# Optimization experiments

Hardware: AMD Instinct MI355X
Metric: run time of the kernel (lower is better)

The kernel has to match this reference:

```python
import jax, jax.numpy as jnp
import numpy as np

K = 5  # k_for_maxpool
EPS_OH = 1.0 - 0.001


def _conv_block(x, W, b):
    # x: [N, L, D]; Conv1d(D, D, 3, padding=2), LeakyReLU(0.1), slice [1:1+L], residual
    L = x.shape[1]
    xc = jnp.swapaxes(x, 1, 2)  # [N, D, L]
    y = jax.lax.conv_general_dilated(xc, W, window_strides=(1,), padding=[(2, 2)],
                                     dimension_numbers=('NCH', 'OIH', 'NCH'))
    y = y + b[None, :, None]
    y = jax.nn.leaky_relu(y, 0.1)
    y = y[:, :, 1:1 + L]
    return jnp.swapaxes(y, 1, 2) + x


def _normalize(x):
    return x / jnp.linalg.norm(x, axis=-1, keepdims=True)


def _pool(sim):
    # sim: [..., Q, L] -> [..., Q, 3]: (max, mean of top-K, mean over all)
    s = jnp.sort(sim, axis=-1)
    kmax = s[..., -K:]
    return jnp.stack([kmax[..., -1], kmax.mean(-1), s.mean(-1)], axis=-1)


def setup_inputs() -> dict:
    key = jax.random.key(0)
    ks = jax.random.split(key, 16)
    S, L, Q, D = 4096, 64, 32, 300
    inp = {
        'doc_sents_embeds': jax.random.normal(ks[0], (S, L, D), jnp.float32),
        'question_embeds': jax.random.normal(ks[1], (Q, D), jnp.float32),
        'q_idfs': jax.random.uniform(ks[2], (Q, 1), jnp.float32),
        'sents_gaf': jax.random.uniform(ks[3], (S, 3), jnp.float32),
        'conv1_w': jax.random.normal(ks[4], (D, D, 3), jnp.float32) * 0.05,
        'conv1_b': jax.random.normal(ks[5], (D,), jnp.float32) * 0.05,
        'conv2_w': jax.random.normal(ks[6], (D, D, 3), jnp.float32) * 0.05,
        'conv2_b': jax.random.normal(ks[7], (D,), jnp.float32) * 0.05,
        'qw_w': jax.random.normal(ks[8], (1, D + 1), jnp.float32) * 0.05,
        'qw_b': jax.random.normal(ks[9], (1,), jnp.float32) * 0.05,
        'mlp1_w': jax.random.normal(ks[10], (8, 9), jnp.float32) * 0.3,
        'mlp1_b': jax.random.normal(ks[11], (8,), jnp.float32) * 0.05,
        'mlp2_w': jax.random.normal(ks[12], (1, 8), jnp.float32) * 0.3,
        'mlp2_b': jax.random.normal(ks[13], (1,), jnp.float32) * 0.05,
        'out_w': jax.random.normal(ks[14], (1, 4), jnp.float32) * 0.3,
    }
    return inp


def reference(doc_sents_embeds, question_embeds, q_idfs, sents_gaf,
              conv1_w, conv1_b, conv2_w, conv2_b,
              qw_w, qw_b, mlp1_w, mlp1_b, mlp2_w, mlp2_b, out_w):
    Q = question_embeds.shape[0]
    # question context (two trigram conv blocks)
    q_ctx = _conv_block(_conv_block(question_embeds[None], conv1_w, conv1_b),
                        conv2_w, conv2_b)[0]  # [Q, D]
    # question token weights
    qw_in = jnp.concatenate([q_ctx, q_idfs], axis=-1)  # [Q, D+1]
    q_weights = jax.nn.softmax((qw_in @ qw_w.T + qw_b)[:, 0], axis=-1)  # [Q]
    # sentence context features, vectorized over all sentences
    sent_ctx = _conv_block(_conv_block(doc_sents_embeds, conv1_w, conv1_b),
                           conv2_w, conv2_b)  # [S, L, D]
    # cosine similarity matrices: [S, Q, L]
    qn = _normalize(question_embeds)
    dn = _normalize(doc_sents_embeds)
    sim_insens = jnp.einsum('qd,sld->sql', qn, dn)
    sim_oh = (sim_insens > EPS_OH).astype(sim_insens.dtype)
    qcn = _normalize(q_ctx)
    scn = _normalize(sent_ctx)
    sim_sens = jnp.einsum('qd,sld->sql', qcn, scn)
    # pooled features: [S, Q, 9] (order: oh, insensitive, sensitive)
    pooled = jnp.concatenate([_pool(sim_oh), _pool(sim_insens), _pool(sim_sens)], axis=-1)
    lo = jax.nn.leaky_relu(pooled @ mlp1_w.T + mlp1_b, 0.1)
    lo = (lo @ mlp2_w.T + mlp2_b)[..., 0]  # [S, Q]
    sent_emit = (lo * q_weights[None, :]).sum(-1) / Q  # [S]
    feats = jnp.concatenate([sents_gaf, sent_emit[:, None]], axis=-1)  # [S, 4]
    return jax.nn.sigmoid(feats @ out_w[0])  # [S]
```

## Files before the change

kernel.cpp:

```cpp
#include <hip/hip_runtime.h>
#include <math.h>

typedef __attribute__((ext_vector_type(8))) short short8;
typedef __attribute__((ext_vector_type(4))) short short4_t;
typedef __attribute__((ext_vector_type(4))) float f32x4;

#define RS      312
#define SST     69
#define EPS_OH  0.999f

__device__ __forceinline__ float waveSum(float v) {
#pragma unroll
  for (int off = 32; off; off >>= 1) v += __shfl_xor(v, off);
  return v;
}
__device__ __forceinline__ float leaky(float x) { return fmaxf(x, 0.1f * x); }

__device__ __forceinline__ short f2b(float f) {
  unsigned u = __float_as_uint(f);
  unsigned r = (u + 0x7FFFu + ((u >> 16) & 1u)) >> 16;
  return (short)r;
}
__device__ __forceinline__ float b2f(short h) {
  return __uint_as_float(((unsigned)(unsigned short)h) << 16);
}

__global__ __launch_bounds__(256) void qconv_kernel(
    const float* __restrict__ x, const float* __restrict__ W,
    const float* __restrict__ b, float* __restrict__ y)
{
  int idx = blockIdx.x * 256 + threadIdx.x;
  if (idx >= 76800) return;
  int part = idx & 7, gid = idx >> 3;
  int o = gid % 300, l = gid / 300;
  const float* Wo = W + o * 900;
  float acc = 0.f;
  for (int i = part; i < 300; i += 8) {
    float x1 = x[l * 300 + i];
    float x0 = (l >= 1) ? x[(l - 1) * 300 + i] : 0.f;
    float x2 = (l <= 30) ? x[(l + 1) * 300 + i] : 0.f;
    acc += Wo[i * 3] * x0 + Wo[i * 3 + 1] * x1 + Wo[i * 3 + 2] * x2;
  }
  acc += __shfl_xor(acc, 1);
  acc += __shfl_xor(acc, 2);
  acc += __shfl_xor(acc, 4);
  if (part == 0) y[gid] = leaky(acc + b[o]) + x[gid];
}

__global__ __launch_bounds__(256) void qfinish_kernel(
    const float* __restrict__ qemb, const float* __restrict__ qctx,
    const float* __restrict__ qidf, const float* __restrict__ qww,
    const float* __restrict__ qwb,
    float* __restrict__ qwv, short* __restrict__ qf)
{
  __shared__ float inq[32], inqc[32], lg[32];
  int tid = threadIdx.x, lane = tid & 63, w = tid >> 6;
  int r = w * 8 + (lane >> 3), sub = lane & 7;
  float sq = 0.f, sqc = 0.f, dt = 0.f;
  for (int i = sub; i < 300; i += 8) {
    float a = qemb[r * 300 + i]; sq  += a * a;
    float c = qctx[r * 300 + i]; sqc += c * c;
    dt += c * qww[i];
  }
#pragma unroll
  for (int off = 4; off; off >>= 1) {
    sq  += __shfl_xor(sq, off);
    sqc += __shfl_xor(sqc, off);
    dt  += __shfl_xor(dt, off);
  }
  if (sub == 0) {
    inq[r] = rsqrtf(sq); inqc[r] = rsqrtf(sqc);
    lg[r] = dt + qidf[r] * qww[300] + qwb[0];
  }
  __syncthreads();
  if (w == 0) {
    float L = (lane < 32) ? lg[lane] : -1e30f;
    float m = L;
#pragma unroll
    for (int off = 32; off; off >>= 1) m = fmaxf(m, __shfl_xor(m, off));
    float e = (lane < 32) ? expf(L - m) : 0.f;
    float ssum = e;
#pragma unroll
    for (int off = 32; off; off >>= 1) ssum += __shfl_xor(ssum, off);
    if (lane < 32) qwv[lane] = e / ssum;
  }
  __syncthreads();
  for (int t = tid; t < 2560; t += 256) {
    int ln = t & 63;
    int rest = t >> 6;
    int kt = rest % 10; rest /= 10;
    int mt = rest & 1; int sflag = rest >> 1;
    const float* src  = sflag ? qctx : qemb;
    const float* innv = sflag ? inqc : inq;
    int q  = mt * 16 + (ln & 15);
    int i0 = kt * 32 + (ln >> 4) * 8;
    float iv = innv[q];
    short8 v;
#pragma unroll
    for (int j = 0; j < 8; ++j) {
      int i = i0 + j;
      v[j] = f2b((i < 300) ? src[q * 300 + i] * iv : 0.f);
    }
    *(short8*)(qf + (size_t)t * 8) = v;
  }
}

__global__ __launch_bounds__(256) void wfrag_kernel(
    const float* __restrict__ W, short* __restrict__ Wf)
{
  int t = blockIdx.x * 256 + threadIdx.x;
  if (t >= 38400) return;
  int lane = t & 63;
  int rest = t >> 6;
  int mt = rest % 20; rest /= 20;
  int kt = rest % 10; int tap = rest / 10;
  int o  = mt * 16 + (lane & 15);
  int i0 = kt * 32 + (lane >> 4) * 8;
  short8 v;
#pragma unroll
  for (int j = 0; j < 8; ++j) {
    int i = i0 + j;
    v[j] = f2b((o < 300 && i < 300) ? W[o * 900 + i * 3 + tap] : 0.f);
  }
  *(short8*)(Wf + (size_t)t * 8) = v;
}


__device__ __forceinline__ void pool_all(
    const float* SIMb, float* featb, int lane, int foff, bool do_oh)
{
  int q = lane >> 1, half = lane & 1;
  const float* p = SIMb + q * SST + half * 32;
  float t0 = -3e38f, t1 = -3e38f, t2 = -3e38f, t3 = -3e38f, t4 = -3e38f;
  float ssum = 0.f;
  int cnt = 0;
#pragma unroll
  for (int i = 0; i < 32; ++i) {
    float v = p[i];
    ssum += v;
    if (do_oh) cnt += (v > EPS_OH) ? 1 : 0;
    float m, c;
    m = fmaxf(t0, v); c = fminf(t0, v); t0 = m;
    m = fmaxf(t1, c); c = fminf(t1, c); t1 = m;
    m = fmaxf(t2, c); c = fminf(t2, c); t2 = m;
    m = fmaxf(t3, c); c = fminf(t3, c); t3 = m;
    t4 = fmaxf(t4, c);
  }
  float p0 = __shfl_xor(t0, 1), p1 = __shfl_xor(t1, 1), p2 = __shfl_xor(t2, 1),
        p3 = __shfl_xor(t3, 1), p4 = __shfl_xor(t4, 1);
  float s2 = __shfl_xor(ssum, 1);
  int   c2 = __shfl_xor(cnt, 1);
  float m0 = fmaxf(t0, p4), m1 = fmaxf(t1, p3), m2 = fmaxf(t2, p2),
        m3 = fmaxf(t3, p1), m4 = fmaxf(t4, p0);
  if (half == 0) {
    float tmax = fmaxf(t0, p0);
    float t5   = m0 + m1 + m2 + m3 + m4;
    float stot = ssum + s2;
    int   c    = cnt + c2;
    float* fq = featb + q * 9;
    if (do_oh) {
      fq[0] = (c > 0) ? 1.f : 0.f;
      fq[1] = (c < 5 ? (float)c : 5.f) * 0.2f;
      fq[2] = (float)c * (1.f / 64.f);
    }
    fq[foff + 0] = tmax;
    fq[foff + 1] = t5 * 0.2f;
    fq[foff + 2] = stot * (1.f / 64.f);
  }
}

__device__ __forceinline__ void conv_mfma_ip3(
    short* tb, const short* __restrict__ Wf,
    const float* __restrict__ bias, int w, int r, int g, int lane)
{
  f32x4 acc[2][4];
#pragma unroll
  for (int mi = 0; mi < 2; ++mi)
#pragma unroll
    for (int nt = 0; nt < 4; ++nt) acc[mi][nt] = (f32x4){0.f, 0.f, 0.f, 0.f};

  const int rm0 = (r == 0) ? 0 : (r - 1);
  const int rp3 = (r == 15) ? 63 : (49 + r);
  int rows[3][4];
  rows[0][0] = rm0;    rows[0][1] = 15 + r; rows[0][2] = 31 + r; rows[0][3] = 47 + r;
  rows[1][0] = r;      rows[1][1] = 16 + r; rows[1][2] = 32 + r; rows[1][3] = 48 + r;
  rows[2][0] = 1 + r;  rows[2][1] = 17 + r; rows[2][2] = 33 + r; rows[2][3] = rp3;

  const short* wl = Wf + (size_t)lane * 8 + (size_t)(2 * w) * 512;
  const int colg = g * 8;

  short8 afb[2][2], bfb[2][4];

#pragma unroll
  for (int mi = 0; mi < 2; ++mi)
    afb[0][mi] = *(const short8*)(wl + (size_t)mi * 512);
#pragma unroll
  for (int nt = 0; nt < 4; ++nt)
    bfb[0][nt] = *(const short8*)(tb + rows[0][nt] * RS + colg);

#pragma unroll
  for (int s = 0; s < 30; ++s) {
    const int kt = s / 3, tap = s % 3;
    const int cur = s & 1, nxt = cur ^ 1;
    if (s + 1 < 30) {
      const int kt2 = (s + 1) / 3, tap2 = (s + 1) % 3;
      const size_t afo = (size_t)((tap2 * 10 + kt2) * 20) * 512;
#pragma unroll
      for (int mi = 0; mi < 2; ++mi)
        afb[nxt][mi] = *(const short8*)(wl + afo + (size_t)mi * 512);
      const int col2 = kt2 * 32 + colg;
#pragma unroll
      for (int nt = 0; nt < 4; ++nt)
        bfb[nxt][nt] = *(const short8*)(tb + rows[tap2][nt] * RS + col2);
    }
    short8 f0 = bfb[cur][0], f1 = bfb[cur][1], f2 = bfb[cur][2], f3 = bfb[cur][3];
    if (tap == 0) f0 = (r == 0)  ? (short8)0 : f0;
    if (tap == 2) f3 = (r == 15) ? (short8)0 : f3;
#pragma unroll
    for (int mi = 0; mi < 2; ++mi) {
      short8 af = afb[cur][mi];
      acc[mi][0] = __builtin_amdgcn_mfma_f32_16x16x32_bf16(af, f0, acc[mi][0], 0, 0, 0);
      acc[mi][1] = __builtin_amdgcn_mfma_f32_16x16x32_bf16(af, f1, acc[mi][1], 0, 0, 0);
      acc[mi][2] = __builtin_amdgcn_mfma_f32_16x16x32_bf16(af, f2, acc[mi][2], 0, 0, 0);
      acc[mi][3] = __builtin_amdgcn_mfma_f32_16x16x32_bf16(af, f3, acc[mi][3], 0, 0, 0);
    }
  }

  f32x4 bv[2];
  short4_t resv[2][4];
#pragma unroll
  for (int mi = 0; mi < 2; ++mi) {
    const int m0 = (w * 2 + mi) * 16 + g * 4;
    if (m0 < 300) {
      bv[mi] = *(const f32x4*)(bias + m0);
#pragma unroll
      for (int nt = 0; nt < 4; ++nt)
        resv[mi][nt] = *(const short4_t*)(tb + (nt * 16 + r) * RS + m0);
    }
  }
  __syncthreads();
#pragma unroll
  for (int mi = 0; mi < 2; ++mi) {
    const int m0 = (w * 2 + mi) * 16 + g * 4;
    if (m0 < 300) {
#pragma unroll
      for (int nt = 0; nt < 4; ++nt) {
        int l = nt * 16 + r;
        short4_t outv;
#pragma unroll
        for (int j = 0; j < 4; ++j) {
          float a = acc[mi][nt][j] + bv[mi][j];
          a = leaky(a) + b2f(resv[mi][nt][j]);
          outv[j] = f2b(a);
        }
        *(short4_t*)(tb + l * RS + m0) = outv;
      }
    }
  }
}

__device__ __forceinline__ void sim_mfma(
    const short* src, const short* __restrict__ qf, const float* invn,
    float* SIMb, int ti, int r, int g, int lane)
{
  int smt = ti >> 2, snt = ti & 3;
  f32x4 acc = (f32x4){0.f, 0.f, 0.f, 0.f};
#pragma unroll
  for (int kt = 0; kt < 10; ++kt) {
    short8 bf = *(const short8*)(src + (snt * 16 + r) * RS + kt * 32 + g * 8);
    short8 af = *(const short8*)(qf + (size_t)((smt * 10 + kt) * 64 + lane) * 8);
    acc = __builtin_amdgcn_mfma_f32_16x16x32_bf16(af, bf, acc, 0, 0, 0);
  }
  int l = snt * 16 + r;
  float iv = invn[l];
#pragma unroll
  for (int j = 0; j < 4; ++j)
    SIMb[(smt * 16 + g * 4 + j) * SST + l] = acc[j] * iv;
}

__device__ __forceinline__ void norms_lds(const short* Xb, float* invn, int tid) {
  if (tid >= 512) return;
  int row = tid >> 3, part = tid & 7;
  float ssum = 0.f;
  for (int i = part * 8; i < 304; i += 64) {
    short8 hv = *(const short8*)(Xb + row * RS + i);
#pragma unroll
    for (int j = 0; j < 8; ++j) { float f = b2f(hv[j]); ssum += f * f; }
  }
  ssum += __shfl_xor(ssum, 1);
  ssum += __shfl_xor(ssum, 2);
  ssum += __shfl_xor(ssum, 4);
  if (part == 0) invn[row] = rsqrtf(ssum);
}

__global__ __launch_bounds__(640, 5) void sent_kernel(
    const float* __restrict__ doc, const short* __restrict__ qf,
    const float* __restrict__ qwv, const float* __restrict__ gaf,
    const short* __restrict__ Wf1, const float* __restrict__ b1,
    const short* __restrict__ Wf2, const float* __restrict__ b2,
    const float* __restrict__ m1w, const float* __restrict__ m1b,
    const float* __restrict__ m2w, const float* __restrict__ m2b,
    const float* __restrict__ ow, float* __restrict__ out)
{
  __shared__ short TB[64 * RS + 8];
  __shared__ float SIMb[32 * SST];
  __shared__ float invn[64];
  __shared__ float featb[288];

  const int tid = threadIdx.x, lane = tid & 63, w = tid >> 6;
  const int r = lane & 15, g = lane >> 4;
  const int s = blockIdx.x;

  if (tid >= 576) {
    short* p = TB + (tid - 576) * RS + 300;
    *(short4_t*)p = (short4_t)0;
    *(short8*)(p + 4) = (short8)0;
  } else if (tid == 575) {
    *(short8*)(TB + 64 * RS) = (short8)0;
  }
  if (tid < 512) {
    int l = tid >> 3, part = tid & 7;
    const float* xr = doc + (size_t)s * 19200 + l * 300;
    float ssum = 0.f;
#pragma unroll
    for (int m = 0; m < 5; ++m) {
      int c = part * 8 + m * 64;
      if (c <= 292) {
        f32x4 u0 = *(const f32x4*)(xr + c);
        f32x4 u1 = *(const f32x4*)(xr + c + 4);
        short8 o;
#pragma unroll
        for (int j = 0; j < 4; ++j) {
          ssum += u0[j] * u0[j] + u1[j] * u1[j];
          o[j] = f2b(u0[j]); o[4 + j] = f2b(u1[j]);
        }
        *(short8*)(TB + l * RS + c) = o;
      } else if (c == 296) {
        f32x4 u0 = *(const f32x4*)(xr + 296);
        short4_t o;
#pragma unroll
        for (int j = 0; j < 4; ++j) { ssum += u0[j] * u0[j]; o[j] = f2b(u0[j]); }
        *(short4_t*)(TB + l * RS + 296) = o;
      }
    }
    ssum += __shfl_xor(ssum, 1);
    ssum += __shfl_xor(ssum, 2);
    ssum += __shfl_xor(ssum, 4);
    if (part == 0) invn[l] = rsqrtf(ssum);
  }
  __syncthreads();

  if (w < 8) sim_mfma(TB, qf, invn, SIMb, w, r, g, lane);
  __syncthreads();

  if (w == 8) pool_all(SIMb, featb, lane, 3, true);
  __syncthreads();

  conv_mfma_ip3(TB, Wf1, b1, w, r, g, lane);
  __syncthreads();

  conv_mfma_ip3(TB, Wf2, b2, w, r, g, lane);
  __syncthreads();

  norms_lds(TB, invn, tid);
  __syncthreads();

  if (w < 8) sim_mfma(TB, qf + 10240, invn, SIMb, w, r, g, lane);
  __syncthreads();

  if (w == 9) pool_all(SIMb, featb, lane, 6, false);
  __syncthreads();

  if (w == 0) {
    float val = 0.f;
    if (lane < 32) {
      int q = lane;
      float o8 = m2b[0];
#pragma unroll
      for (int j = 0; j < 8; ++j) {
        float a = m1b[j];
#pragma unroll
        for (int f = 0; f < 9; ++f) a += m1w[j * 9 + f] * featb[q * 9 + f];
        a = leaky(a);
        o8 += m2w[j] * a;
      }
      val = o8 * qwv[q];
    }
    float tot = waveSum(val);
    if (lane == 0) {
      float emit = tot * (1.f / 32.f);
      float z = gaf[s * 3 + 0] * ow[0] + gaf[s * 3 + 1] * ow[1] +
                gaf[s * 3 + 2] * ow[2] + emit * ow[3];
      out[s] = 1.f / (1.f + expf(-z));
    }
  }
}

extern "C" void kernel_launch(void* const* d_in, const int* in_sizes, int n_in,
                              void* d_out, int out_size, void* d_ws, size_t ws_size,
                              hipStream_t stream)
{
  const float* doc  = (const float*)d_in[0];
  const float* qemb = (const float*)d_in[1];
  const float* qidf = (const float*)d_in[2];
  const float* gaf  = (const float*)d_in[3];
  const float* W1   = (const float*)d_in[4];
  const float* b1   = (const float*)d_in[5];
  const float* W2   = (const float*)d_in[6];
  const float* b2   = (const float*)d_in[7];
  const float* qww  = (const float*)d_in[8];
  const float* qwb  = (const float*)d_in[9];
  const float* m1w  = (const float*)d_in[10];
  const float* m1b  = (const float*)d_in[11];
  const float* m2w  = (const float*)d_in[12];
  const float* m2b  = (const float*)d_in[13];
  const float* ow   = (const float*)d_in[14];
  float* out = (float*)d_out;

  float* ws   = (float*)d_ws;
  float* qc1  = ws;
  float* qctx = ws + 9600;
  float* qwv  = ws + 19200;
  short* wsS  = (short*)(ws + 19232);
  short* Wf1  = wsS;
  short* Wf2  = wsS + 307200;
  short* qfS  = wsS + 614400;

  wfrag_kernel<<<150, 256, 0, stream>>>(W1, Wf1);
  wfrag_kernel<<<150, 256, 0, stream>>>(W2, Wf2);
  qconv_kernel<<<300, 256, 0, stream>>>(qemb, W1, b1, qc1);
  qconv_kernel<<<300, 256, 0, stream>>>(qc1, W2, b2, qctx);
  qfinish_kernel<<<1, 256, 0, stream>>>(qemb, qctx, qidf, qww, qwb, qwv, qfS);
  sent_kernel<<<4096, 640, 0, stream>>>(doc, qfS, qwv, gaf, Wf1, b1, Wf2, b2,
                                        m1w, m1b, m2w, m2b, ow, out);
}
```

Measured before the change: 545.2 us.

## Shrink sentence block to 8 waves with uneven conv M-tile split

Cuts the per-sentence block from 10 waves (640 threads) to 8 waves (512 threads). The 20 conv output M-tiles are now split so waves 0-2 take three tiles each and waves 3-7 take two, and the pooling passes move to waves 6 and 7. The aim is to remove two mostly idle waves and allow more blocks per CU. In exchange, the waves with three tiles hold more accumulator registers and take longer, which makes the conv stage imbalanced.

```diff
diff --git a/kernel.cpp b/kernel.cpp
--- a/kernel.cpp
+++ b/kernel.cpp
@@ -169,13 +169,14 @@
   }
 }
 
+template <int NMT>
 __device__ __forceinline__ void conv_mfma_ip3(
     short* tb, const short* __restrict__ Wf,
-    const float* __restrict__ bias, int w, int r, int g, int lane)
-{
-  f32x4 acc[2][4];
-#pragma unroll
-  for (int mi = 0; mi < 2; ++mi)
+    const float* __restrict__ bias, int base, int r, int g, int lane)
+{
+  f32x4 acc[NMT][4];
+#pragma unroll
+  for (int mi = 0; mi < NMT; ++mi)
 #pragma unroll
     for (int nt = 0; nt < 4; ++nt) acc[mi][nt] = (f32x4){0.f, 0.f, 0.f, 0.f};
 
@@ -186,13 +187,13 @@
   rows[1][0] = r;      rows[1][1] = 16 + r; rows[1][2] = 32 + r; rows[1][3] = 48 + r;
   rows[2][0] = 1 + r;  rows[2][1] = 17 + r; rows[2][2] = 33 + r; rows[2][3] = rp3;
 
-  const short* wl = Wf + (size_t)lane * 8 + (size_t)(2 * w) * 512;
+  const short* wl = Wf + (size_t)lane * 8 + (size_t)base * 512;
   const int colg = g * 8;
 
-  short8 afb[2][2], bfb[2][4];
-
-#pragma unroll
-  for (int mi = 0; mi < 2; ++mi)
+  short8 afb[2][NMT], bfb[2][4];
+
+#pragma unroll
+  for (int mi = 0; mi < NMT; ++mi)
     afb[0][mi] = *(const short8*)(wl + (size_t)mi * 512);
 #pragma unroll
   for (int nt = 0; nt < 4; ++nt)
@@ -206,7 +207,7 @@
       const int kt2 = (s + 1) / 3, tap2 = (s + 1) % 3;
       const size_t afo = (size_t)((tap2 * 10 + kt2) * 20) * 512;
 #pragma unroll
-      for (int mi = 0; mi < 2; ++mi)
+      for (int mi = 0; mi < NMT; ++mi)
         afb[nxt][mi] = *(const short8*)(wl + afo + (size_t)mi * 512);
       const int col2 = kt2 * 32 + colg;
 #pragma unroll
@@ -217,7 +218,7 @@
     if (tap == 0) f0 = (r == 0)  ? (short8)0 : f0;
     if (tap == 2) f3 = (r == 15) ? (short8)0 : f3;
 #pragma unroll
-    for (int mi = 0; mi < 2; ++mi) {
+    for (int mi = 0; mi < NMT; ++mi) {
       short8 af = afb[cur][mi];
       acc[mi][0] = __builtin_amdgcn_mfma_f32_16x16x32_bf16(af, f0, acc[mi][0], 0, 0, 0);
       acc[mi][1] = __builtin_amdgcn_mfma_f32_16x16x32_bf16(af, f1, acc[mi][1], 0, 0, 0);
@@ -226,11 +227,11 @@
     }
   }
 
-  f32x4 bv[2];
-  short4_t resv[2][4];
-#pragma unroll
-  for (int mi = 0; mi < 2; ++mi) {
-    const int m0 = (w * 2 + mi) * 16 + g * 4;
+  f32x4 bv[NMT];
+  short4_t resv[NMT][4];
+#pragma unroll
+  for (int mi = 0; mi < NMT; ++mi) {
+    const int m0 = (base + mi) * 16 + g * 4;
     if (m0 < 300) {
       bv[mi] = *(const f32x4*)(bias + m0);
 #pragma unroll
@@ -240,8 +241,8 @@
   }
   __syncthreads();
 #pragma unroll
-  for (int mi = 0; mi < 2; ++mi) {
-    const int m0 = (w * 2 + mi) * 16 + g * 4;
+  for (int mi = 0; mi < NMT; ++mi) {
+    const int m0 = (base + mi) * 16 + g * 4;
     if (m0 < 300) {
 #pragma unroll
       for (int nt = 0; nt < 4; ++nt) {
@@ -279,7 +280,6 @@
 }
 
 __device__ __forceinline__ void norms_lds(const short* Xb, float* invn, int tid) {
-  if (tid >= 512) return;
   int row = tid >> 3, part = tid & 7;
   float ssum = 0.f;
   for (int i = part * 8; i < 304; i += 64) {
@@ -293,7 +293,7 @@
   if (part == 0) invn[row] = rsqrtf(ssum);
 }
 
-__global__ __launch_bounds__(640, 5) void sent_kernel(
+__global__ __launch_bounds__(512, 4) void sent_kernel(
     const float* __restrict__ doc, const short* __restrict__ qf,
     const float* __restrict__ qwv, const float* __restrict__ gaf,
     const short* __restrict__ Wf1, const float* __restrict__ b1,
@@ -311,14 +311,13 @@
   const int r = lane & 15, g = lane >> 4;
   const int s = blockIdx.x;
 
-  if (tid >= 576) {
-    short* p = TB + (tid - 576) * RS + 300;
+  if (tid < 64) {
+    short* p = TB + tid * RS + 300;
     *(short4_t*)p = (short4_t)0;
     *(short8*)(p + 4) = (short8)0;
-  } else if (tid == 575) {
-    *(short8*)(TB + 64 * RS) = (short8)0;
-  }
-  if (tid < 512) {
+    if (tid == 0) *(short8*)(TB + 64 * RS) = (short8)0;
+  }
+  {
     int l = tid >> 3, part = tid & 7;
     const float* xr = doc + (size_t)s * 19200 + l * 300;
     float ssum = 0.f;
@@ -350,25 +349,27 @@
   }
   __syncthreads();
 
-  if (w < 8) sim_mfma(TB, qf, invn, SIMb, w, r, g, lane);
-  __syncthreads();
-
-  if (w == 8) pool_all(SIMb, featb, lane, 3, true);
-  __syncthreads();
-
-  conv_mfma_ip3(TB, Wf1, b1, w, r, g, lane);
-  __syncthreads();
-
-  conv_mfma_ip3(TB, Wf2, b2, w, r, g, lane);
+  sim_mfma(TB, qf, invn, SIMb, w, r, g, lane);
+  __syncthreads();
+
+  if (w == 6) pool_all(SIMb, featb, lane, 3, true);
+  __syncthreads();
+
+  if (w < 3) conv_mfma_ip3<3>(TB, Wf1, b1, 3 * w, r, g, lane);
+  else       conv_mfma_ip3<2>(TB, Wf1, b1, 2 * w + 3, r, g, lane);
+  __syncthreads();
+
+  if (w < 3) conv_mfma_ip3<3>(TB, Wf2, b2, 3 * w, r, g, lane);
+  else       conv_mfma_ip3<2>(TB, Wf2, b2, 2 * w + 3, r, g, lane);
   __syncthreads();
 
   norms_lds(TB, invn, tid);
   __syncthreads();
 
-  if (w < 8) sim_mfma(TB, qf + 10240, invn, SIMb, w, r, g, lane);
-  __syncthreads();
-
-  if (w == 9) pool_all(SIMb, featb, lane, 6, false);
+  sim_mfma(TB, qf + 10240, invn, SIMb, w, r, g, lane);
+  __syncthreads();
+
+  if (w == 7) pool_all(SIMb, featb, lane, 6, false);
   __syncthreads();
 
   if (w == 0) {
@@ -431,6 +432,6 @@
   qconv_kernel<<<300, 256, 0, stream>>>(qemb, W1, b1, qc1);
   qconv_kernel<<<300, 256, 0, stream>>>(qc1, W2, b2, qctx);
   qfinish_kernel<<<1, 256, 0, stream>>>(qemb, qctx, qidf, qww, qwb, qwv, qfS);
-  sent_kernel<<<4096, 640, 0, stream>>>(doc, qfS, qwv, gaf, Wf1, b1, Wf2, b2,
+  sent_kernel<<<4096, 512, 0, stream>>>(doc, qfS, qwv, gaf, Wf1, b1, Wf2, b2,
                                         m1w, m1b, m2w, m2b, ow, out);
 }
```

New measurement: 472.6 us. 13.3% less time.
